# Optimization experiments

Measured on AMD Instinct MI355X. Metric: run time of the kernel, lower is better.

The kernel has to match this reference:

```python
import jax, jax.numpy as jnp
import numpy as np

EMB = 768

def _mlp2(x, Wa, Wb):
    # relu(LL2(relu(LL1(x)))), bias-free linears stored as [out, in]
    return jax.nn.relu(jax.nn.relu(x @ Wa.T) @ Wb.T)

def setup_inputs() -> dict:
    key = jax.random.key(0)
    ks = jax.random.split(key, 6)
    n, m = 16, 4096  # maxlen = 64 paragraphs -> 64*64 pair slots
    X_data = jax.random.normal(ks[0], (n, 1 + m, 3 * EMB), dtype=jnp.float32)
    # first token carries num_clusters metadata (unused by the differentiable path)
    W1 = jax.random.normal(ks[1], (256, EMB), dtype=jnp.float32) * 0.02
    W2 = jax.random.normal(ks[2], (128, 256), dtype=jnp.float32) * 0.02
    W3 = jax.random.normal(ks[3], (256, EMB), dtype=jnp.float32) * 0.02
    W4 = jax.random.normal(ks[4], (128, 256), dtype=jnp.float32) * 0.02
    W5 = jax.random.normal(ks[5], (1, 128), dtype=jnp.float32) * 0.02
    return {"X_data": X_data, "W1": W1, "W2": W2, "W3": W3, "W4": W4, "W5": W5}

def reference(X_data, W1, W2, W3, W4, W5):
    # CATSCluster differentiable path: QueryScaler on X_data[:, 1:, :]
    X = X_data[:, 1:, :]                      # [n, m, 3*EMB]
    Xq = X[..., :EMB]
    Xp1 = X[..., EMB:2 * EMB]
    Xp2 = X[..., 2 * EMB:]
    Xp1z = _mlp2(Xp1, W1, W2)                 # [n, m, 128]
    Xp2z = _mlp2(Xp2, W1, W2)
    Xqz = _mlp2(Xq, W3, W4)
    Xpqz = Xqz * jnp.abs(Xp1z - Xp2z)         # [n, m, 128]
    dist = jnp.tanh(jax.nn.relu(Xpqz @ W5.T))[..., 0]  # [n, m]
    n, m = dist.shape
    p = int(np.sqrt(m))                       # maxlen
    # batch_pairscore_matrix fed to the host-side clustering step
    return dist.reshape(n, p, p)
```

## Files before the change

### kernel.cpp

```cpp
#include <hip/hip_runtime.h>


typedef short short8 __attribute__((ext_vector_type(8)));
typedef float f32x4 __attribute__((ext_vector_type(4)));

#define W1H_OFF 0u
#define W1L_OFF 196608u
#define W3H_OFF 393216u
#define W3L_OFF 589824u
#define W2H_OFF 786432u
#define W2L_OFF 819200u
#define W4H_OFF 851968u
#define W4L_OFF 884736u

__device__ __forceinline__ unsigned short bf16_rne(float f) {
  unsigned int u = __float_as_uint(f);
  u += 0x7FFFu + ((u >> 16) & 1u);
  return (unsigned short)(u >> 16);
}

__device__ __forceinline__ void split_bf16(float f, unsigned short& h, unsigned short& l) {
  h = bf16_rne(f);
  float fh = __uint_as_float(((unsigned int)h) << 16);
  l = bf16_rne(f - fh);
}

__device__ __forceinline__ void pack_split4(const float4 v, uint2& ph, uint2& pl) {
  unsigned short h0,h1,h2,h3,l0,l1,l2,l3;
  split_bf16(v.x,h0,l0); split_bf16(v.y,h1,l1);
  split_bf16(v.z,h2,l2); split_bf16(v.w,h3,l3);
  ph.x = (unsigned)h0 | ((unsigned)h1 << 16); ph.y = (unsigned)h2 | ((unsigned)h3 << 16);
  pl.x = (unsigned)l0 | ((unsigned)l1 << 16); pl.y = (unsigned)l2 | ((unsigned)l3 << 16);
}

__global__ __launch_bounds__(256) void prep_weights(
    const float* __restrict__ W1, const float* __restrict__ W2,
    const float* __restrict__ W3, const float* __restrict__ W4,
    unsigned short* __restrict__ ws)
{
  int i = blockIdx.x * 256 + threadIdx.x;
  if (i < 196608) {
    unsigned short h, l;
    split_bf16(W1[i], h, l); ws[W1H_OFF + i] = h; ws[W1L_OFF + i] = l;
    split_bf16(W3[i], h, l); ws[W3H_OFF + i] = h; ws[W3L_OFF + i] = l;
    if (i < 32768) {
      split_bf16(W2[i], h, l); ws[W2H_OFF + i] = h; ws[W2L_OFF + i] = l;
      split_bf16(W4[i], h, l); ws[W4H_OFF + i] = h; ws[W4L_OFF + i] = l;
    }
  }
}

#define STRIDE_A 72
#define STRIDE_H 264

__global__ __launch_bounds__(512, 4) void catsc_main(
    const float* __restrict__ X, const unsigned short* __restrict__ ws,
    const float* __restrict__ W5, float* __restrict__ out)
{
  __shared__ short lsA[2][2][64 * STRIDE_A];
  __shared__ short lsH[64 * STRIDE_H];
  __shared__ float lsPart[8][64];

  const int tid  = threadIdx.x;
  const int wave = tid >> 6;
  const int lane = tid & 63;
  const int l15  = lane & 15;
  const int q    = lane >> 4;
  const int blk  = blockIdx.x;

  const float* Xb = X + (size_t)((blk >> 6) * 4097 + 1 + ((blk & 63) << 6)) * 2304;

  const int srow = tid >> 3;
  const int scol = (tid & 7) << 3;
  const float* Xs = Xb + (size_t)srow * 2304 + scol;
  short* lsW = &lsA[0][0][0];
  const int sidx = srow * STRIDE_A + scol;
  const int PLANE = 64 * STRIDE_A;

  const int arow = l15 * STRIDE_A + q * 8;
  const size_t bwl = (size_t)(wave * 32 + l15) * 768 + q * 8;
  const size_t cwl = (size_t)(wave * 16 + l15) * 256 + q * 8;
  const int hrow = l15 * STRIDE_H + q * 8;

  f32x4 zp[4];

  float4 vP0 = *(const float4*)(Xs + 768);
  float4 vP1 = *(const float4*)(Xs + 768 + 4);

#pragma unroll 1
  for (int s = 0; s < 3; ++s) {
    const int so = (s == 0) ? 768 : (s == 1) ? 1536 : 0;
    const unsigned short* B1h = ws + (s == 2 ? W3H_OFF : W1H_OFF) + bwl;
    const unsigned short* B2h = ws + (s == 2 ? W4H_OFF : W2H_OFF) + cwl;

    f32x4 acc[4][2];
#pragma unroll
    for (int m = 0; m < 4; ++m)
#pragma unroll
      for (int n = 0; n < 2; ++n)
        acc[m][n] = f32x4{0.f, 0.f, 0.f, 0.f};

    {
      uint2 ph, pl;
      pack_split4(vP0, ph, pl);
      *(uint2*)&lsW[sidx]         = ph;
      *(uint2*)&lsW[PLANE + sidx] = pl;
      pack_split4(vP1, ph, pl);
      *(uint2*)&lsW[sidx + 4]         = ph;
      *(uint2*)&lsW[PLANE + sidx + 4] = pl;
    }
    __syncthreads();

    for (int p = 0; p < 12; ++p) {
      const int b = p & 1;
      float4 vB0, vB1;
      if (p + 1 < 12) {
        vB0 = *(const float4*)(Xs + so + (p + 1) * 64);
        vB1 = *(const float4*)(Xs + so + (p + 1) * 64 + 4);
      }
      const short* As0 = &lsA[b][0][arow];
      const short* As1 = &lsA[b][1][arow];

#pragma unroll
      for (int sub = 0; sub < 2; ++sub) {
#pragma unroll
        for (int mh = 0; mh < 2; ++mh) {
          short8 Ah[2], Al[2];
#pragma unroll
          for (int mm = 0; mm < 2; ++mm) {
            const int a = (mh * 2 + mm) * 16 * STRIDE_A + sub * 32;
            Ah[mm] = *(const short8*)(As0 + a);
            Al[mm] = *(const short8*)(As1 + a);
          }
#pragma unroll
          for (int n = 0; n < 2; ++n) {
            const unsigned short* bp = B1h + (size_t)n * 12288 + p * 64 + sub * 32;
            short8 Bh = *(const short8*)bp;
            short8 Bl = *(const short8*)(bp + 196608);
            acc[mh*2+0][n] = __builtin_amdgcn_mfma_f32_16x16x32_bf16(Ah[0], Bh, acc[mh*2+0][n], 0, 0, 0);
            acc[mh*2+1][n] = __builtin_amdgcn_mfma_f32_16x16x32_bf16(Ah[1], Bh, acc[mh*2+1][n], 0, 0, 0);
            acc[mh*2+0][n] = __builtin_amdgcn_mfma_f32_16x16x32_bf16(Ah[0], Bl, acc[mh*2+0][n], 0, 0, 0);
            acc[mh*2+1][n] = __builtin_amdgcn_mfma_f32_16x16x32_bf16(Ah[1], Bl, acc[mh*2+1][n], 0, 0, 0);
            acc[mh*2+0][n] = __builtin_amdgcn_mfma_f32_16x16x32_bf16(Al[0], Bh, acc[mh*2+0][n], 0, 0, 0);
            acc[mh*2+1][n] = __builtin_amdgcn_mfma_f32_16x16x32_bf16(Al[1], Bh, acc[mh*2+1][n], 0, 0, 0);
          }
        }
      }

      if (p + 1 < 12) {
        short* dst = lsW + (b ^ 1) * (2 * PLANE);
        uint2 ph, pl;
        pack_split4(vB0, ph, pl);
        *(uint2*)&dst[sidx]         = ph;
        *(uint2*)&dst[PLANE + sidx] = pl;
        pack_split4(vB1, ph, pl);
        *(uint2*)&dst[sidx + 4]         = ph;
        *(uint2*)&dst[PLANE + sidx + 4] = pl;
      }
      __syncthreads();
    }

#pragma unroll
    for (int m = 0; m < 4; ++m)
#pragma unroll
      for (int n = 0; n < 2; ++n) {
        int col = (wave * 2 + n) * 16 + l15;
#pragma unroll
        for (int i = 0; i < 4; ++i) {
          int row = m * 16 + q * 4 + i;
          lsH[row * STRIDE_H + col] = bf16_rne(fmaxf(acc[m][n][i], 0.f));
        }
      }
    __syncthreads();

    if (s < 2) {
      const int nso = (s == 0) ? 1536 : 0;
      vP0 = *(const float4*)(Xs + nso);
      vP1 = *(const float4*)(Xs + nso + 4);
    }

    f32x4 acc2[4];
#pragma unroll
    for (int m = 0; m < 4; ++m) acc2[m] = f32x4{0.f, 0.f, 0.f, 0.f};

    for (int c2 = 0; c2 < 8; ++c2) {
      const unsigned short* cp = B2h + c2 * 32;
      short8 Ch = *(const short8*)cp;
      short8 Cl = *(const short8*)(cp + 32768);
      short8 Ha[4];
#pragma unroll
      for (int m = 0; m < 4; ++m)
        Ha[m] = *(const short8*)&lsH[m * 16 * STRIDE_H + hrow + c2 * 32];
#pragma unroll
      for (int m = 0; m < 4; ++m)
        acc2[m] = __builtin_amdgcn_mfma_f32_16x16x32_bf16(Ha[m], Ch, acc2[m], 0, 0, 0);
#pragma unroll
      for (int m = 0; m < 4; ++m)
        acc2[m] = __builtin_amdgcn_mfma_f32_16x16x32_bf16(Ha[m], Cl, acc2[m], 0, 0, 0);
    }

    if (s == 0) {
#pragma unroll
      for (int m = 0; m < 4; ++m)
#pragma unroll
        for (int i = 0; i < 4; ++i)
          zp[m][i] = fmaxf(acc2[m][i], 0.f);
    } else if (s == 1) {
#pragma unroll
      for (int m = 0; m < 4; ++m)
#pragma unroll
        for (int i = 0; i < 4; ++i)
          zp[m][i] = fabsf(zp[m][i] - fmaxf(acc2[m][i], 0.f));
    } else {
      const float w5c = W5[wave * 16 + l15];
#pragma unroll
      for (int m = 0; m < 4; ++m)
#pragma unroll
        for (int i = 0; i < 4; ++i) {
          float v = fmaxf(acc2[m][i], 0.f) * zp[m][i] * w5c;
          v += __shfl_xor(v, 1);
          v += __shfl_xor(v, 2);
          v += __shfl_xor(v, 4);
          v += __shfl_xor(v, 8);
          if (l15 == 0) lsPart[wave][m * 16 + q * 4 + i] = v;
        }
    }
  }

  __syncthreads();
  if (tid < 64) {
    float sum = lsPart[0][tid] + lsPart[1][tid] + lsPart[2][tid] + lsPart[3][tid]
              + lsPart[4][tid] + lsPart[5][tid] + lsPart[6][tid] + lsPart[7][tid];
    out[(size_t)blk * 64 + tid] = tanhf(fmaxf(sum, 0.f));
  }
}

extern "C" void kernel_launch(void* const* d_in, const int* in_sizes, int n_in,
                              void* d_out, int out_size, void* d_ws, size_t ws_size,
                              hipStream_t stream) {
  const float* X  = (const float*)d_in[0];
  const float* W1 = (const float*)d_in[1];
  const float* W2 = (const float*)d_in[2];
  const float* W3 = (const float*)d_in[3];
  const float* W4 = (const float*)d_in[4];
  const float* W5 = (const float*)d_in[5];
  float* out = (float*)d_out;
  unsigned short* ws = (unsigned short*)d_ws;

  prep_weights<<<dim3(768), dim3(256), 0, stream>>>(W1, W2, W3, W4, ws);
  catsc_main<<<dim3(1024), dim3(512), 0, stream>>>(X, ws, W5, out);
}
```

Before: 1.032 ms.

## Halve row tile to 32 with 4 waves and prefetch B fragments

```diff
diff --git a/kernel.cpp b/kernel.cpp
--- a/kernel.cpp
+++ b/kernel.cpp
@@ -53,13 +53,13 @@
 #define STRIDE_A 72
 #define STRIDE_H 264
 
-__global__ __launch_bounds__(512, 4) void catsc_main(
+__global__ __launch_bounds__(256, 4) void catsc_main(
     const float* __restrict__ X, const unsigned short* __restrict__ ws,
     const float* __restrict__ W5, float* __restrict__ out)
 {
-  __shared__ short lsA[2][2][64 * STRIDE_A];
-  __shared__ short lsH[64 * STRIDE_H];
-  __shared__ float lsPart[8][64];
+  __shared__ short lsA[2][2][32 * STRIDE_A];
+  __shared__ short lsH[32 * STRIDE_H];
+  __shared__ float lsPart[4][32];
 
   const int tid  = threadIdx.x;
   const int wave = tid >> 6;
@@ -68,21 +68,21 @@
   const int q    = lane >> 4;
   const int blk  = blockIdx.x;
 
-  const float* Xb = X + (size_t)((blk >> 6) * 4097 + 1 + ((blk & 63) << 6)) * 2304;
+  const float* Xb = X + (size_t)((blk >> 7) * 4097 + 1 + ((blk & 127) << 5)) * 2304;
 
   const int srow = tid >> 3;
   const int scol = (tid & 7) << 3;
   const float* Xs = Xb + (size_t)srow * 2304 + scol;
   short* lsW = &lsA[0][0][0];
   const int sidx = srow * STRIDE_A + scol;
-  const int PLANE = 64 * STRIDE_A;
+  const int PLANE = 32 * STRIDE_A;
 
   const int arow = l15 * STRIDE_A + q * 8;
-  const size_t bwl = (size_t)(wave * 32 + l15) * 768 + q * 8;
-  const size_t cwl = (size_t)(wave * 16 + l15) * 256 + q * 8;
+  const size_t bwl = (size_t)(wave * 64 + l15) * 768 + q * 8;
+  const size_t cwl = (size_t)(wave * 32 + l15) * 256 + q * 8;
   const int hrow = l15 * STRIDE_H + q * 8;
 
-  f32x4 zp[4];
+  f32x4 zp[2][2];
 
   float4 vP0 = *(const float4*)(Xs + 768);
   float4 vP1 = *(const float4*)(Xs + 768 + 4);
@@ -93,11 +93,11 @@
     const unsigned short* B1h = ws + (s == 2 ? W3H_OFF : W1H_OFF) + bwl;
     const unsigned short* B2h = ws + (s == 2 ? W4H_OFF : W2H_OFF) + cwl;
 
-    f32x4 acc[4][2];
-#pragma unroll
-    for (int m = 0; m < 4; ++m)
-#pragma unroll
-      for (int n = 0; n < 2; ++n)
+    f32x4 acc[2][4];
+#pragma unroll
+    for (int m = 0; m < 2; ++m)
+#pragma unroll
+      for (int n = 0; n < 4; ++n)
         acc[m][n] = f32x4{0.f, 0.f, 0.f, 0.f};
 
     {
@@ -123,28 +123,34 @@
 
 #pragma unroll
       for (int sub = 0; sub < 2; ++sub) {
-#pragma unroll
-        for (int mh = 0; mh < 2; ++mh) {
-          short8 Ah[2], Al[2];
-#pragma unroll
-          for (int mm = 0; mm < 2; ++mm) {
-            const int a = (mh * 2 + mm) * 16 * STRIDE_A + sub * 32;
-            Ah[mm] = *(const short8*)(As0 + a);
-            Al[mm] = *(const short8*)(As1 + a);
+        short8 Ah[2], Al[2];
+#pragma unroll
+        for (int mm = 0; mm < 2; ++mm) {
+          const int a = mm * 16 * STRIDE_A + sub * 32;
+          Ah[mm] = *(const short8*)(As0 + a);
+          Al[mm] = *(const short8*)(As1 + a);
+        }
+        const unsigned short* bp0 = B1h + p * 64 + sub * 32;
+        short8 Bh = *(const short8*)bp0;
+        short8 Bl = *(const short8*)(bp0 + 196608);
+        __builtin_amdgcn_s_setprio(1);
+#pragma unroll
+        for (int n = 0; n < 4; ++n) {
+          short8 BhN, BlN;
+          if (n < 3) {
+            const unsigned short* bp = B1h + (size_t)(n + 1) * 12288 + p * 64 + sub * 32;
+            BhN = *(const short8*)bp;
+            BlN = *(const short8*)(bp + 196608);
           }
-#pragma unroll
-          for (int n = 0; n < 2; ++n) {
-            const unsigned short* bp = B1h + (size_t)n * 12288 + p * 64 + sub * 32;
-            short8 Bh = *(const short8*)bp;
-            short8 Bl = *(const short8*)(bp + 196608);
-            acc[mh*2+0][n] = __builtin_amdgcn_mfma_f32_16x16x32_bf16(Ah[0], Bh, acc[mh*2+0][n], 0, 0, 0);
-            acc[mh*2+1][n] = __builtin_amdgcn_mfma_f32_16x16x32_bf16(Ah[1], Bh, acc[mh*2+1][n], 0, 0, 0);
-            acc[mh*2+0][n] = __builtin_amdgcn_mfma_f32_16x16x32_bf16(Ah[0], Bl, acc[mh*2+0][n], 0, 0, 0);
-            acc[mh*2+1][n] = __builtin_amdgcn_mfma_f32_16x16x32_bf16(Ah[1], Bl, acc[mh*2+1][n], 0, 0, 0);
-            acc[mh*2+0][n] = __builtin_amdgcn_mfma_f32_16x16x32_bf16(Al[0], Bh, acc[mh*2+0][n], 0, 0, 0);
-            acc[mh*2+1][n] = __builtin_amdgcn_mfma_f32_16x16x32_bf16(Al[1], Bh, acc[mh*2+1][n], 0, 0, 0);
-          }
-        }
+          acc[0][n] = __builtin_amdgcn_mfma_f32_16x16x32_bf16(Ah[0], Bh, acc[0][n], 0, 0, 0);
+          acc[1][n] = __builtin_amdgcn_mfma_f32_16x16x32_bf16(Ah[1], Bh, acc[1][n], 0, 0, 0);
+          acc[0][n] = __builtin_amdgcn_mfma_f32_16x16x32_bf16(Ah[0], Bl, acc[0][n], 0, 0, 0);
+          acc[1][n] = __builtin_amdgcn_mfma_f32_16x16x32_bf16(Ah[1], Bl, acc[1][n], 0, 0, 0);
+          acc[0][n] = __builtin_amdgcn_mfma_f32_16x16x32_bf16(Al[0], Bh, acc[0][n], 0, 0, 0);
+          acc[1][n] = __builtin_amdgcn_mfma_f32_16x16x32_bf16(Al[1], Bh, acc[1][n], 0, 0, 0);
+          Bh = BhN; Bl = BlN;
+        }
+        __builtin_amdgcn_s_setprio(0);
       }
 
       if (p + 1 < 12) {
@@ -161,10 +167,10 @@
     }
 
 #pragma unroll
-    for (int m = 0; m < 4; ++m)
-#pragma unroll
-      for (int n = 0; n < 2; ++n) {
-        int col = (wave * 2 + n) * 16 + l15;
+    for (int m = 0; m < 2; ++m)
+#pragma unroll
+      for (int n = 0; n < 4; ++n) {
+        int col = (wave * 4 + n) * 16 + l15;
 #pragma unroll
         for (int i = 0; i < 4; ++i) {
           int row = m * 16 + q * 4 + i;
@@ -179,45 +185,55 @@
       vP1 = *(const float4*)(Xs + nso + 4);
     }
 
-    f32x4 acc2[4];
-#pragma unroll
-    for (int m = 0; m < 4; ++m) acc2[m] = f32x4{0.f, 0.f, 0.f, 0.f};
+    f32x4 acc2[2][2];
+#pragma unroll
+    for (int m = 0; m < 2; ++m)
+#pragma unroll
+      for (int n2 = 0; n2 < 2; ++n2)
+        acc2[m][n2] = f32x4{0.f, 0.f, 0.f, 0.f};
 
     for (int c2 = 0; c2 < 8; ++c2) {
-      const unsigned short* cp = B2h + c2 * 32;
-      short8 Ch = *(const short8*)cp;
-      short8 Cl = *(const short8*)(cp + 32768);
-      short8 Ha[4];
-#pragma unroll
-      for (int m = 0; m < 4; ++m)
+      short8 Ha[2];
+#pragma unroll
+      for (int m = 0; m < 2; ++m)
         Ha[m] = *(const short8*)&lsH[m * 16 * STRIDE_H + hrow + c2 * 32];
 #pragma unroll
-      for (int m = 0; m < 4; ++m)
-        acc2[m] = __builtin_amdgcn_mfma_f32_16x16x32_bf16(Ha[m], Ch, acc2[m], 0, 0, 0);
-#pragma unroll
-      for (int m = 0; m < 4; ++m)
-        acc2[m] = __builtin_amdgcn_mfma_f32_16x16x32_bf16(Ha[m], Cl, acc2[m], 0, 0, 0);
+      for (int n2 = 0; n2 < 2; ++n2) {
+        const unsigned short* cp = B2h + n2 * 4096 + c2 * 32;
+        short8 Ch = *(const short8*)cp;
+        short8 Cl = *(const short8*)(cp + 32768);
+        acc2[0][n2] = __builtin_amdgcn_mfma_f32_16x16x32_bf16(Ha[0], Ch, acc2[0][n2], 0, 0, 0);
+        acc2[1][n2] = __builtin_amdgcn_mfma_f32_16x16x32_bf16(Ha[1], Ch, acc2[1][n2], 0, 0, 0);
+        acc2[0][n2] = __builtin_amdgcn_mfma_f32_16x16x32_bf16(Ha[0], Cl, acc2[0][n2], 0, 0, 0);
+        acc2[1][n2] = __builtin_amdgcn_mfma_f32_16x16x32_bf16(Ha[1], Cl, acc2[1][n2], 0, 0, 0);
+      }
     }
 
     if (s == 0) {
 #pragma unroll
-      for (int m = 0; m < 4; ++m)
-#pragma unroll
-        for (int i = 0; i < 4; ++i)
-          zp[m][i] = fmaxf(acc2[m][i], 0.f);
+      for (int m = 0; m < 2; ++m)
+#pragma unroll
+        for (int n2 = 0; n2 < 2; ++n2)
+#pragma unroll
+          for (int i = 0; i < 4; ++i)
+            zp[m][n2][i] = fmaxf(acc2[m][n2][i], 0.f);
     } else if (s == 1) {
 #pragma unroll
-      for (int m = 0; m < 4; ++m)
-#pragma unroll
-        for (int i = 0; i < 4; ++i)
-          zp[m][i] = fabsf(zp[m][i] - fmaxf(acc2[m][i], 0.f));
+      for (int m = 0; m < 2; ++m)
+#pragma unroll
+        for (int n2 = 0; n2 < 2; ++n2)
+#pragma unroll
+          for (int i = 0; i < 4; ++i)
+            zp[m][n2][i] = fabsf(zp[m][n2][i] - fmaxf(acc2[m][n2][i], 0.f));
     } else {
-      const float w5c = W5[wave * 16 + l15];
-#pragma unroll
-      for (int m = 0; m < 4; ++m)
+      const float w5c0 = W5[wave * 32 + l15];
+      const float w5c1 = W5[wave * 32 + 16 + l15];
+#pragma unroll
+      for (int m = 0; m < 2; ++m)
 #pragma unroll
         for (int i = 0; i < 4; ++i) {
-          float v = fmaxf(acc2[m][i], 0.f) * zp[m][i] * w5c;
+          float v = fmaxf(acc2[m][0][i], 0.f) * zp[m][0][i] * w5c0
+                  + fmaxf(acc2[m][1][i], 0.f) * zp[m][1][i] * w5c1;
           v += __shfl_xor(v, 1);
           v += __shfl_xor(v, 2);
           v += __shfl_xor(v, 4);
@@ -228,10 +244,9 @@
   }
 
   __syncthreads();
-  if (tid < 64) {
-    float sum = lsPart[0][tid] + lsPart[1][tid] + lsPart[2][tid] + lsPart[3][tid]
-              + lsPart[4][tid] + lsPart[5][tid] + lsPart[6][tid] + lsPart[7][tid];
-    out[(size_t)blk * 64 + tid] = tanhf(fmaxf(sum, 0.f));
+  if (tid < 32) {
+    float sum = lsPart[0][tid] + lsPart[1][tid] + lsPart[2][tid] + lsPart[3][tid];
+    out[(size_t)blk * 32 + tid] = tanhf(fmaxf(sum, 0.f));
   }
 }
 
@@ -248,5 +263,5 @@
   unsigned short* ws = (unsigned short*)d_ws;
 
   prep_weights<<<dim3(768), dim3(256), 0, stream>>>(W1, W2, W3, W4, ws);
-  catsc_main<<<dim3(1024), dim3(512), 0, stream>>>(X, ws, W5, out);
-}
+  catsc_main<<<dim3(2048), dim3(256), 0, stream>>>(X, ws, W5, out);
+}
```

Result: slower. 1.292 ms (+25.1%).

## Fuse the two paragraph-branch first-layer GEMMs to share W1 fragment loads

Applied to the files above, without the earlier changes.

```diff
diff --git a/kernel.cpp b/kernel.cpp
--- a/kernel.cpp
+++ b/kernel.cpp
@@ -50,15 +50,20 @@
   }
 }
 
-#define STRIDE_A 72
-#define STRIDE_H 264
+#define SA32 40
+#define P32  (64 * SA32)
+#define SA64 72
+#define P64  (64 * SA64)
+#define SH   264
+#define HSZ  (64 * SH)
+
+#define SMEM_SHORTS 35328
 
 __global__ __launch_bounds__(512, 4) void catsc_main(
     const float* __restrict__ X, const unsigned short* __restrict__ ws,
     const float* __restrict__ W5, float* __restrict__ out)
 {
-  __shared__ short lsA[2][2][64 * STRIDE_A];
-  __shared__ short lsH[64 * STRIDE_H];
+  __shared__ short smem[SMEM_SHORTS];
   __shared__ float lsPart[8][64];
 
   const int tid  = threadIdx.x;
@@ -71,162 +76,229 @@
   const float* Xb = X + (size_t)((blk >> 6) * 4097 + 1 + ((blk & 63) << 6)) * 2304;
 
   const int srow = tid >> 3;
-  const int scol = (tid & 7) << 3;
-  const float* Xs = Xb + (size_t)srow * 2304 + scol;
-  short* lsW = &lsA[0][0][0];
-  const int sidx = srow * STRIDE_A + scol;
-  const int PLANE = 64 * STRIDE_A;
-
-  const int arow = l15 * STRIDE_A + q * 8;
+  const int c32  = (tid & 7) << 2;
+  const int c64  = (tid & 7) << 3;
+  const float* Xs = Xb + (size_t)srow * 2304;
+  const int si32 = srow * SA32 + c32;
+  const int si64 = srow * SA64 + c64;
+
+  const int arow32 = l15 * SA32 + q * 8;
+  const int arow64 = l15 * SA64 + q * 8;
   const size_t bwl = (size_t)(wave * 32 + l15) * 768 + q * 8;
   const size_t cwl = (size_t)(wave * 16 + l15) * 256 + q * 8;
-  const int hrow = l15 * STRIDE_H + q * 8;
-
-  f32x4 zp[4];
-
-  float4 vP0 = *(const float4*)(Xs + 768);
-  float4 vP1 = *(const float4*)(Xs + 768 + 4);
-
-#pragma unroll 1
-  for (int s = 0; s < 3; ++s) {
-    const int so = (s == 0) ? 768 : (s == 1) ? 1536 : 0;
-    const unsigned short* B1h = ws + (s == 2 ? W3H_OFF : W1H_OFF) + bwl;
-    const unsigned short* B2h = ws + (s == 2 ? W4H_OFF : W2H_OFF) + cwl;
-
-    f32x4 acc[4][2];
+  const int hrow = l15 * SH + q * 8;
+
+  const unsigned short* W1b = ws + W1H_OFF + bwl;
+  const unsigned short* W3b = ws + W3H_OFF + bwl;
+  const unsigned short* W2b = ws + W2H_OFF + cwl;
+  const unsigned short* W4b = ws + W4H_OFF + cwl;
+
+  auto storeH = [&](f32x4 (&a)[4][2]) {
 #pragma unroll
     for (int m = 0; m < 4; ++m)
 #pragma unroll
-      for (int n = 0; n < 2; ++n)
-        acc[m][n] = f32x4{0.f, 0.f, 0.f, 0.f};
-
-    {
-      uint2 ph, pl;
-      pack_split4(vP0, ph, pl);
-      *(uint2*)&lsW[sidx]         = ph;
-      *(uint2*)&lsW[PLANE + sidx] = pl;
-      pack_split4(vP1, ph, pl);
-      *(uint2*)&lsW[sidx + 4]         = ph;
-      *(uint2*)&lsW[PLANE + sidx + 4] = pl;
-    }
-    __syncthreads();
-
-    for (int p = 0; p < 12; ++p) {
-      const int b = p & 1;
-      float4 vB0, vB1;
-      if (p + 1 < 12) {
-        vB0 = *(const float4*)(Xs + so + (p + 1) * 64);
-        vB1 = *(const float4*)(Xs + so + (p + 1) * 64 + 4);
+      for (int n = 0; n < 2; ++n) {
+        const int col = wave * 32 + n * 16 + l15;
+#pragma unroll
+        for (int i = 0; i < 4; ++i)
+          smem[(m * 16 + q * 4 + i) * SH + col] = bf16_rne(fmaxf(a[m][n][i], 0.f));
       }
-      const short* As0 = &lsA[b][0][arow];
-      const short* As1 = &lsA[b][1][arow];
-
-#pragma unroll
-      for (int sub = 0; sub < 2; ++sub) {
-#pragma unroll
-        for (int mh = 0; mh < 2; ++mh) {
-          short8 Ah[2], Al[2];
-#pragma unroll
-          for (int mm = 0; mm < 2; ++mm) {
-            const int a = (mh * 2 + mm) * 16 * STRIDE_A + sub * 32;
-            Ah[mm] = *(const short8*)(As0 + a);
-            Al[mm] = *(const short8*)(As1 + a);
-          }
-#pragma unroll
-          for (int n = 0; n < 2; ++n) {
-            const unsigned short* bp = B1h + (size_t)n * 12288 + p * 64 + sub * 32;
-            short8 Bh = *(const short8*)bp;
-            short8 Bl = *(const short8*)(bp + 196608);
-            acc[mh*2+0][n] = __builtin_amdgcn_mfma_f32_16x16x32_bf16(Ah[0], Bh, acc[mh*2+0][n], 0, 0, 0);
-            acc[mh*2+1][n] = __builtin_amdgcn_mfma_f32_16x16x32_bf16(Ah[1], Bh, acc[mh*2+1][n], 0, 0, 0);
-            acc[mh*2+0][n] = __builtin_amdgcn_mfma_f32_16x16x32_bf16(Ah[0], Bl, acc[mh*2+0][n], 0, 0, 0);
-            acc[mh*2+1][n] = __builtin_amdgcn_mfma_f32_16x16x32_bf16(Ah[1], Bl, acc[mh*2+1][n], 0, 0, 0);
-            acc[mh*2+0][n] = __builtin_amdgcn_mfma_f32_16x16x32_bf16(Al[0], Bh, acc[mh*2+0][n], 0, 0, 0);
-            acc[mh*2+1][n] = __builtin_amdgcn_mfma_f32_16x16x32_bf16(Al[1], Bh, acc[mh*2+1][n], 0, 0, 0);
-          }
-        }
-      }
-
-      if (p + 1 < 12) {
-        short* dst = lsW + (b ^ 1) * (2 * PLANE);
-        uint2 ph, pl;
-        pack_split4(vB0, ph, pl);
-        *(uint2*)&dst[sidx]         = ph;
-        *(uint2*)&dst[PLANE + sidx] = pl;
-        pack_split4(vB1, ph, pl);
-        *(uint2*)&dst[sidx + 4]         = ph;
-        *(uint2*)&dst[PLANE + sidx + 4] = pl;
-      }
-      __syncthreads();
-    }
-
-#pragma unroll
-    for (int m = 0; m < 4; ++m)
-#pragma unroll
-      for (int n = 0; n < 2; ++n) {
-        int col = (wave * 2 + n) * 16 + l15;
-#pragma unroll
-        for (int i = 0; i < 4; ++i) {
-          int row = m * 16 + q * 4 + i;
-          lsH[row * STRIDE_H + col] = bf16_rne(fmaxf(acc[m][n][i], 0.f));
-        }
-      }
-    __syncthreads();
-
-    if (s < 2) {
-      const int nso = (s == 0) ? 1536 : 0;
-      vP0 = *(const float4*)(Xs + nso);
-      vP1 = *(const float4*)(Xs + nso + 4);
-    }
-
-    f32x4 acc2[4];
-#pragma unroll
-    for (int m = 0; m < 4; ++m) acc2[m] = f32x4{0.f, 0.f, 0.f, 0.f};
-
+  };
+
+  auto gemm2 = [&](const unsigned short* Cb, f32x4 (&o)[4]) {
+#pragma unroll
+    for (int m = 0; m < 4; ++m) o[m] = f32x4{0.f, 0.f, 0.f, 0.f};
     for (int c2 = 0; c2 < 8; ++c2) {
-      const unsigned short* cp = B2h + c2 * 32;
+      const unsigned short* cp = Cb + c2 * 32;
       short8 Ch = *(const short8*)cp;
       short8 Cl = *(const short8*)(cp + 32768);
       short8 Ha[4];
 #pragma unroll
       for (int m = 0; m < 4; ++m)
-        Ha[m] = *(const short8*)&lsH[m * 16 * STRIDE_H + hrow + c2 * 32];
+        Ha[m] = *(const short8*)&smem[m * 16 * SH + hrow + c2 * 32];
 #pragma unroll
       for (int m = 0; m < 4; ++m)
-        acc2[m] = __builtin_amdgcn_mfma_f32_16x16x32_bf16(Ha[m], Ch, acc2[m], 0, 0, 0);
+        o[m] = __builtin_amdgcn_mfma_f32_16x16x32_bf16(Ha[m], Ch, o[m], 0, 0, 0);
 #pragma unroll
       for (int m = 0; m < 4; ++m)
-        acc2[m] = __builtin_amdgcn_mfma_f32_16x16x32_bf16(Ha[m], Cl, acc2[m], 0, 0, 0);
-    }
-
-    if (s == 0) {
-#pragma unroll
-      for (int m = 0; m < 4; ++m)
-#pragma unroll
-        for (int i = 0; i < 4; ++i)
-          zp[m][i] = fmaxf(acc2[m][i], 0.f);
-    } else if (s == 1) {
-#pragma unroll
-      for (int m = 0; m < 4; ++m)
-#pragma unroll
-        for (int i = 0; i < 4; ++i)
-          zp[m][i] = fabsf(zp[m][i] - fmaxf(acc2[m][i], 0.f));
-    } else {
-      const float w5c = W5[wave * 16 + l15];
-#pragma unroll
-      for (int m = 0; m < 4; ++m)
-#pragma unroll
-        for (int i = 0; i < 4; ++i) {
-          float v = fmaxf(acc2[m][i], 0.f) * zp[m][i] * w5c;
-          v += __shfl_xor(v, 1);
-          v += __shfl_xor(v, 2);
-          v += __shfl_xor(v, 4);
-          v += __shfl_xor(v, 8);
-          if (l15 == 0) lsPart[wave][m * 16 + q * 4 + i] = v;
+        o[m] = __builtin_amdgcn_mfma_f32_16x16x32_bf16(Ha[m], Cl, o[m], 0, 0, 0);
+    }
+  };
+
+  f32x4 acc[2][4][2];
+#pragma unroll
+  for (int t = 0; t < 2; ++t)
+#pragma unroll
+    for (int m = 0; m < 4; ++m)
+#pragma unroll
+      for (int n = 0; n < 2; ++n)
+        acc[t][m][n] = f32x4{0.f, 0.f, 0.f, 0.f};
+
+  {
+    float4 vF0 = *(const float4*)(Xs + 768 + c32);
+    float4 vF1 = *(const float4*)(Xs + 1536 + c32);
+    uint2 ph, pl;
+    pack_split4(vF0, ph, pl);
+    *(uint2*)&smem[si32]       = ph; *(uint2*)&smem[P32 + si32]     = pl;
+    pack_split4(vF1, ph, pl);
+    *(uint2*)&smem[2*P32+si32] = ph; *(uint2*)&smem[3*P32 + si32]   = pl;
+  }
+  __syncthreads();
+
+#pragma unroll 1
+  for (int p = 0; p < 24; ++p) {
+    const int b = p & 1;
+    float4 v0, v1;
+    if (p + 1 < 24) {
+      v0 = *(const float4*)(Xs + 768  + (p + 1) * 32 + c32);
+      v1 = *(const float4*)(Xs + 1536 + (p + 1) * 32 + c32);
+    }
+    const short* Ab = smem + b * (4 * P32);
+
+#pragma unroll
+    for (int n = 0; n < 2; ++n) {
+      const unsigned short* bp = W1b + n * 12288 + p * 32;
+      short8 Bh = *(const short8*)bp;
+      short8 Bl = *(const short8*)(bp + 196608);
+#pragma unroll
+      for (int t = 0; t < 2; ++t) {
+        const short* a0 = Ab + t * (2 * P32) + arow32;
+#pragma unroll
+        for (int mh = 0; mh < 2; ++mh) {
+          short8 Ah[2], Al[2];
+#pragma unroll
+          for (int mm = 0; mm < 2; ++mm) {
+            const int a = (mh * 2 + mm) * 16 * SA32;
+            Ah[mm] = *(const short8*)(a0 + a);
+            Al[mm] = *(const short8*)(a0 + P32 + a);
+          }
+          acc[t][mh*2+0][n] = __builtin_amdgcn_mfma_f32_16x16x32_bf16(Ah[0], Bh, acc[t][mh*2+0][n], 0, 0, 0);
+          acc[t][mh*2+1][n] = __builtin_amdgcn_mfma_f32_16x16x32_bf16(Ah[1], Bh, acc[t][mh*2+1][n], 0, 0, 0);
+          acc[t][mh*2+0][n] = __builtin_amdgcn_mfma_f32_16x16x32_bf16(Ah[0], Bl, acc[t][mh*2+0][n], 0, 0, 0);
+          acc[t][mh*2+1][n] = __builtin_amdgcn_mfma_f32_16x16x32_bf16(Ah[1], Bl, acc[t][mh*2+1][n], 0, 0, 0);
+          acc[t][mh*2+0][n] = __builtin_amdgcn_mfma_f32_16x16x32_bf16(Al[0], Bh, acc[t][mh*2+0][n], 0, 0, 0);
+          acc[t][mh*2+1][n] = __builtin_amdgcn_mfma_f32_16x16x32_bf16(Al[1], Bh, acc[t][mh*2+1][n], 0, 0, 0);
         }
-    }
-  }
-
+      }
+    }
+
+    if (p + 1 < 24) {
+      short* d = smem + (b ^ 1) * (4 * P32);
+      uint2 ph, pl;
+      pack_split4(v0, ph, pl);
+      *(uint2*)&d[si32]           = ph; *(uint2*)&d[P32 + si32]     = pl;
+      pack_split4(v1, ph, pl);
+      *(uint2*)&d[2*P32 + si32]   = ph; *(uint2*)&d[3*P32 + si32]   = pl;
+    }
+    __syncthreads();
+  }
+
+  float4 vQ0 = *(const float4*)(Xs + c64);
+  float4 vQ1 = *(const float4*)(Xs + c64 + 4);
+
+  storeH(acc[0]);
+  __syncthreads();
+
+  f32x4 acc2[4];
+  f32x4 zp[4];
+  gemm2(W2b, acc2);
+  {
+    short* Aq = smem + HSZ;
+    uint2 ph, pl;
+    pack_split4(vQ0, ph, pl);
+    *(uint2*)&Aq[si64]     = ph; *(uint2*)&Aq[P64 + si64]     = pl;
+    pack_split4(vQ1, ph, pl);
+    *(uint2*)&Aq[si64 + 4] = ph; *(uint2*)&Aq[P64 + si64 + 4] = pl;
+  }
+#pragma unroll
+  for (int m = 0; m < 4; ++m)
+#pragma unroll
+    for (int i = 0; i < 4; ++i)
+      zp[m][i] = fmaxf(acc2[m][i], 0.f);
+  __syncthreads();
+
+  storeH(acc[1]);
+  __syncthreads();
+
+  gemm2(W2b, acc2);
+#pragma unroll
+  for (int m = 0; m < 4; ++m)
+#pragma unroll
+    for (int i = 0; i < 4; ++i)
+      zp[m][i] = fabsf(zp[m][i] - fmaxf(acc2[m][i], 0.f));
+
+  f32x4 aq[4][2];
+#pragma unroll
+  for (int m = 0; m < 4; ++m)
+#pragma unroll
+    for (int n = 0; n < 2; ++n)
+      aq[m][n] = f32x4{0.f, 0.f, 0.f, 0.f};
+
+#pragma unroll 1
+  for (int p = 0; p < 12; ++p) {
+    const int b = p & 1;
+    float4 w0, w1;
+    if (p + 1 < 12) {
+      w0 = *(const float4*)(Xs + (p + 1) * 64 + c64);
+      w1 = *(const float4*)(Xs + (p + 1) * 64 + c64 + 4);
+    }
+    const short* A0 = smem + HSZ + b * (2 * P64);
+
+#pragma unroll
+    for (int sub = 0; sub < 2; ++sub) {
+#pragma unroll
+      for (int n = 0; n < 2; ++n) {
+        const unsigned short* bp = W3b + n * 12288 + p * 64 + sub * 32;
+        short8 Bh = *(const short8*)bp;
+        short8 Bl = *(const short8*)(bp + 196608);
+#pragma unroll
+        for (int mh = 0; mh < 2; ++mh) {
+          short8 Ah[2], Al[2];
+#pragma unroll
+          for (int mm = 0; mm < 2; ++mm) {
+            const int a = (mh * 2 + mm) * 16 * SA64 + sub * 32 + arow64;
+            Ah[mm] = *(const short8*)(A0 + a);
+            Al[mm] = *(const short8*)(A0 + P64 + a);
+          }
+          aq[mh*2+0][n] = __builtin_amdgcn_mfma_f32_16x16x32_bf16(Ah[0], Bh, aq[mh*2+0][n], 0, 0, 0);
+          aq[mh*2+1][n] = __builtin_amdgcn_mfma_f32_16x16x32_bf16(Ah[1], Bh, aq[mh*2+1][n], 0, 0, 0);
+          aq[mh*2+0][n] = __builtin_amdgcn_mfma_f32_16x16x32_bf16(Ah[0], Bl, aq[mh*2+0][n], 0, 0, 0);
+          aq[mh*2+1][n] = __builtin_amdgcn_mfma_f32_16x16x32_bf16(Ah[1], Bl, aq[mh*2+1][n], 0, 0, 0);
+          aq[mh*2+0][n] = __builtin_amdgcn_mfma_f32_16x16x32_bf16(Al[0], Bh, aq[mh*2+0][n], 0, 0, 0);
+          aq[mh*2+1][n] = __builtin_amdgcn_mfma_f32_16x16x32_bf16(Al[1], Bh, aq[mh*2+1][n], 0, 0, 0);
+        }
+      }
+    }
+
+    if (p + 1 < 12) {
+      short* d = smem + HSZ + (b ^ 1) * (2 * P64);
+      uint2 ph, pl;
+      pack_split4(w0, ph, pl);
+      *(uint2*)&d[si64]     = ph; *(uint2*)&d[P64 + si64]     = pl;
+      pack_split4(w1, ph, pl);
+      *(uint2*)&d[si64 + 4] = ph; *(uint2*)&d[P64 + si64 + 4] = pl;
+    }
+    __syncthreads();
+  }
+
+  storeH(aq);
+  __syncthreads();
+
+  gemm2(W4b, acc2);
+  {
+    const float w5c = W5[wave * 16 + l15];
+#pragma unroll
+    for (int m = 0; m < 4; ++m)
+#pragma unroll
+      for (int i = 0; i < 4; ++i) {
+        float v = fmaxf(acc2[m][i], 0.f) * zp[m][i] * w5c;
+        v += __shfl_xor(v, 1);
+        v += __shfl_xor(v, 2);
+        v += __shfl_xor(v, 4);
+        v += __shfl_xor(v, 8);
+        if (l15 == 0) lsPart[wave][m * 16 + q * 4 + i] = v;
+      }
+  }
   __syncthreads();
   if (tid < 64) {
     float sum = lsPart[0][tid] + lsPart[1][tid] + lsPart[2][tid] + lsPart[3][tid]
```

Result: slower. 1.387 ms (+34.3%).
